# Optimization experiments

Measured on AMD Instinct MI355X. Metric: run time of the kernel, lower is better.

The kernel has to match this reference:

```python
import jax, jax.numpy as jnp
import numpy as np

EPS = 1e-12  # matches torch F.normalize default eps


def setup_inputs() -> dict:
    key = jax.random.key(0)
    k_x, k_w1, k_b1, k_w2, k_b2 = jax.random.split(key, 5)
    b, n, r, d = 8, 64, 256, 512
    return {
        "x": jax.random.normal(k_x, (b, n, r, d), dtype=jnp.float32),
        "W1": jax.random.normal(k_w1, (d, d), dtype=jnp.float32) * (1.0 / np.sqrt(d)),
        "b1": jax.random.normal(k_b1, (d,), dtype=jnp.float32) * 0.01,
        "W2": jax.random.normal(k_w2, (1, d), dtype=jnp.float32) * (1.0 / np.sqrt(d)),
        "b2": jax.random.normal(k_b2, (1,), dtype=jnp.float32) * 0.01,
    }


def reference(x, W1, b1, W2, b2):
    # F.normalize(x, dim=-1): x / max(||x||_2, eps)
    norm = jnp.sqrt(jnp.sum(x * x, axis=-1, keepdims=True))
    xn = x / jnp.maximum(norm, EPS)                      # [b,n,r,d]
    h = jnp.tanh(jnp.einsum('bnrd,ed->bnre', xn, W1) + b1)  # linear1 + tanh
    scores = (jnp.einsum('bnrd,od->bnro', h, W2) + b2)[..., 0]  # [b,n,r]
    alphas = jax.nn.softmax(scores, axis=2)              # softmax over regions r
    fbar = jnp.einsum('bnr,bnrd->bnd', alphas, xn)       # weighted pooling
    return (fbar, alphas)
```

## Files before the change

kernel.cpp:

```cpp
#include <hip/hip_runtime.h>
#include <hip/hip_bf16.h>

typedef short short8 __attribute__((ext_vector_type(8)));
typedef float floatx4 __attribute__((ext_vector_type(4)));

#define NGROUP 512
#define RREG 256
#define D 512
#define ROWS 131072
#define FBAR_ELEMS (NGROUP * D)

__device__ __forceinline__ unsigned short f2bf(float f) {
    unsigned int u = __float_as_uint(f);
    unsigned int r = (u + 0x7fffu + ((u >> 16) & 1u)) >> 16;
    return (unsigned short)r;
}
__device__ __forceinline__ float fast_tanh(float x) {
    float cx = fminf(fmaxf(x, -9.5f), 9.5f);
    float e  = __builtin_amdgcn_exp2f(cx * 2.8853900817779268f);
    return (e - 1.f) * __builtin_amdgcn_rcpf(e + 1.f);
}

__global__ __launch_bounds__(256) void conv_w1(const float* __restrict__ W1,
                                               unsigned short* __restrict__ W1c) {
    int tid = blockIdx.x * 256 + threadIdx.x;
    int P = tid * 8;
    int kc = P >> 15;
    int L = P & 32767;
    int col = L >> 6;
    int q = L & 63;
    int kl = (q ^ (((col >> 1) & 3) << 4)) >> 1;
    const float* src = W1 + col * 512 + kc * 32 + kl;
    float4 v = *reinterpret_cast<const float4*>(src);
    ushort4 o;
    o.x = f2bf(v.x); o.y = f2bf(v.y); o.z = f2bf(v.z); o.w = f2bf(v.w);
    *reinterpret_cast<ushort4*>((char*)W1c + P) = o;
}

__global__ __launch_bounds__(512, 4) void score_gemm(
    const float* __restrict__ x, const unsigned short* __restrict__ W1c,
    const float* __restrict__ b1, const float* __restrict__ W2v,
    float* __restrict__ inv_norm, float* __restrict__ scores) {

    __shared__ unsigned short A_lds[2][64 * 32];
    __shared__ unsigned short B_lds[2][512 * 32];
    __shared__ float ss_lds[64][8];
    __shared__ float inv_s[64];
    __shared__ float scorebuf[8][64];

    const int t = threadIdx.x;
    const int lane = t & 63;
    const int w = t >> 6;
    const int cl = lane & 15;
    const int hi = lane >> 4;
    const size_t row0 = (size_t)blockIdx.x * 64;

    auto stageB = [&](int buf, int kc) {
        const char* gb = (const char*)W1c + kc * 32768 + w * 4096 + lane * 16;
        char* lb = (char*)B_lds[buf] + w * 4096;
        #pragma unroll
        for (int i = 0; i < 4; ++i) {
            __builtin_amdgcn_global_load_lds(
                (const __attribute__((address_space(1))) void*)(gb + i * 1024),
                (__attribute__((address_space(3))) void*)(lb + i * 1024),
                16, 0, 0);
        }
    };

    const int arow = t >> 3;
    const int abyte = arow * 64 + (((t & 7) * 8) ^ (((arow >> 1) & 3) << 4));
    const float* xbase = x + (row0 + arow) * (size_t)D + (t & 7) * 4;

    float ssacc = 0.f;
    auto packA = [&](int buf, const float4& xv) {
        ssacc += xv.x * xv.x + xv.y * xv.y + xv.z * xv.z + xv.w * xv.w;
        ushort4 pk;
        pk.x = f2bf(xv.x); pk.y = f2bf(xv.y); pk.z = f2bf(xv.z); pk.w = f2bf(xv.w);
        *reinterpret_cast<ushort4*>((char*)A_lds[buf] + abyte) = pk;
    };

    stageB(0, 0);
    {
        float4 xv = *reinterpret_cast<const float4*>(xbase);
        packA(0, xv);
    }
    __syncthreads();

    floatx4 acc[4][4];
    #pragma unroll
    for (int tt = 0; tt < 4; ++tt)
        #pragma unroll
        for (int f = 0; f < 4; ++f) acc[tt][f] = floatx4{0, 0, 0, 0};

    const int fswz = ((cl >> 1) & 3) << 4;
    const int fofs = (hi * 16) ^ fswz;

    #pragma unroll 2
    for (int s = 0; s < 16; ++s) {
        const int cur = s & 1, nx = cur ^ 1;

        float4 xv;
        if (s < 15) {
            xv = *reinterpret_cast<const float4*>(xbase + (s + 1) * 32);
            stageB(nx, s + 1);
        }

        short8 afr[4], bfr[4];
        #pragma unroll
        for (int tt = 0; tt < 4; ++tt)
            afr[tt] = *reinterpret_cast<const short8*>(
                (char*)A_lds[cur] + (tt * 16 + cl) * 64 + fofs);
        #pragma unroll
        for (int f = 0; f < 4; ++f)
            bfr[f] = *reinterpret_cast<const short8*>(
                (char*)B_lds[cur] + (w * 64 + f * 16 + cl) * 64 + fofs);

        #pragma unroll
        for (int tt = 0; tt < 4; ++tt)
            #pragma unroll
            for (int f = 0; f < 4; ++f)
                acc[tt][f] = __builtin_amdgcn_mfma_f32_16x16x32_bf16(
                    afr[tt], bfr[f], acc[tt][f], 0, 0, 0);

        if (s < 15) {
            packA(nx, xv);
            __syncthreads();
        }
    }

    ss_lds[arow][t & 7] = ssacc;
    __syncthreads();
    if (t < 64) {
        float ss = 0.f;
        #pragma unroll
        for (int j = 0; j < 8; ++j) ss += ss_lds[t][j];
        float inv = 1.0f / fmaxf(sqrtf(ss), 1e-12f);
        inv_s[t] = inv;
        inv_norm[row0 + t] = inv;
    }
    __syncthreads();

    float sp[4][4];
    #pragma unroll
    for (int tt = 0; tt < 4; ++tt)
        #pragma unroll
        for (int i = 0; i < 4; ++i) sp[tt][i] = 0.f;

    #pragma unroll
    for (int f = 0; f < 4; ++f) {
        int col = w * 64 + f * 16 + cl;
        float wv = W2v[col];
        float bb = b1[col];
        #pragma unroll
        for (int tt = 0; tt < 4; ++tt) {
            #pragma unroll
            for (int i = 0; i < 4; ++i) {
                float iv = inv_s[tt * 16 + hi * 4 + i];
                sp[tt][i] += wv * fast_tanh(acc[tt][f][i] * iv + bb);
            }
        }
    }

    #pragma unroll
    for (int tt = 0; tt < 4; ++tt) {
        #pragma unroll
        for (int i = 0; i < 4; ++i) {
            float v = sp[tt][i];
            v += __shfl_xor(v, 1, 64);
            v += __shfl_xor(v, 2, 64);
            v += __shfl_xor(v, 4, 64);
            v += __shfl_xor(v, 8, 64);
            if (cl == 0) scorebuf[w][tt * 16 + hi * 4 + i] = v;
        }
    }
    __syncthreads();

    if (t < 64) {
        float s = 0.f;
        #pragma unroll
        for (int q = 0; q < 8; ++q) s += scorebuf[q][t];
        scores[row0 + t] = s;
    }
}

__global__ __launch_bounds__(512) void softmax_pool(
    const float* __restrict__ x, const float* __restrict__ inv_norm,
    const float* __restrict__ scores, float* __restrict__ out) {

    __shared__ float F[RREG];
    __shared__ float wts[RREG];
    const int t = threadIdx.x;
    const int g = blockIdx.x;

    float s = 0.f, e = 0.f;
    if (t < RREG) { s = scores[g * RREG + t]; F[t] = s; }
    __syncthreads();
    for (int off = 128; off > 0; off >>= 1) {
        if (t < off) F[t] = fmaxf(F[t], F[t + off]);
        __syncthreads();
    }
    float mx = F[0];
    __syncthreads();
    if (t < RREG) { e = expf(s - mx); F[t] = e; }
    __syncthreads();
    for (int off = 128; off > 0; off >>= 1) {
        if (t < off) F[t] += F[t + off];
        __syncthreads();
    }
    float denom = F[0];
    if (t < RREG) {
        float al = e / denom;
        out[FBAR_ELEMS + (size_t)g * RREG + t] = al;
        wts[t] = al * inv_norm[(size_t)g * RREG + t];
    }
    __syncthreads();

    float a = 0.f;
    const float* xb = x + (size_t)g * RREG * D + t;
    #pragma unroll 16
    for (int r = 0; r < RREG; ++r) a += wts[r] * xb[(size_t)r * D];
    out[(size_t)g * D + t] = a;
}

extern "C" void kernel_launch(void* const* d_in, const int* in_sizes, int n_in,
                              void* d_out, int out_size, void* d_ws, size_t ws_size,
                              hipStream_t stream) {
    const float* x  = (const float*)d_in[0];
    const float* W1 = (const float*)d_in[1];
    const float* b1 = (const float*)d_in[2];
    const float* w2 = (const float*)d_in[3];
    float* out = (float*)d_out;

    unsigned short* W1c = (unsigned short*)d_ws;
    float* inv_norm = (float*)((char*)d_ws + 524288);
    float* scores   = (float*)((char*)d_ws + 1048576);

    conv_w1<<<256, 256, 0, stream>>>(W1, W1c);
    score_gemm<<<ROWS / 64, 512, 0, stream>>>(x, W1c, b1, w2, inv_norm, scores);
    softmax_pool<<<NGROUP, 512, 0, stream>>>(x, inv_norm, scores, out);
}
```

Before: 160.1 us.

## Double score GEMM block to 1024 threads with 32 columns per wave

The score GEMM block grows from 512 to 1024 threads (16 waves), so each wave now computes 64 rows by 32 columns instead of 64 columns. The A-tile load and the W1 staging are split across twice as many threads. The row sum-of-squares reduction now uses 16-lane shuffles instead of an LDS pass, and the score buffer reuses the A LDS region to save shared memory. The aim is more waves per CU to hide memory latency and fewer registers per thread. The cost is half as many MFMAs per LDS fragment load and more block-wide synchronisation overhead.

```diff
diff --git a/kernel.cpp b/kernel.cpp
--- a/kernel.cpp
+++ b/kernel.cpp
@@ -37,16 +37,14 @@
     *reinterpret_cast<ushort4*>((char*)W1c + P) = o;
 }
 
-__global__ __launch_bounds__(512, 4) void score_gemm(
+__global__ __launch_bounds__(1024, 8) void score_gemm(
     const float* __restrict__ x, const unsigned short* __restrict__ W1c,
     const float* __restrict__ b1, const float* __restrict__ W2v,
     float* __restrict__ inv_norm, float* __restrict__ scores) {
 
     __shared__ unsigned short A_lds[2][64 * 32];
     __shared__ unsigned short B_lds[2][512 * 32];
-    __shared__ float ss_lds[64][8];
     __shared__ float inv_s[64];
-    __shared__ float scorebuf[8][64];
 
     const int t = threadIdx.x;
     const int lane = t & 63;
@@ -56,10 +54,10 @@
     const size_t row0 = (size_t)blockIdx.x * 64;
 
     auto stageB = [&](int buf, int kc) {
-        const char* gb = (const char*)W1c + kc * 32768 + w * 4096 + lane * 16;
-        char* lb = (char*)B_lds[buf] + w * 4096;
-        #pragma unroll
-        for (int i = 0; i < 4; ++i) {
+        const char* gb = (const char*)W1c + kc * 32768 + w * 2048 + lane * 16;
+        char* lb = (char*)B_lds[buf] + w * 2048;
+        #pragma unroll
+        for (int i = 0; i < 2; ++i) {
             __builtin_amdgcn_global_load_lds(
                 (const __attribute__((address_space(1))) void*)(gb + i * 1024),
                 (__attribute__((address_space(3))) void*)(lb + i * 1024),
@@ -67,60 +65,52 @@
         }
     };
 
-    const int arow = t >> 3;
-    const int abyte = arow * 64 + (((t & 7) * 8) ^ (((arow >> 1) & 3) << 4));
-    const float* xbase = x + (row0 + arow) * (size_t)D + (t & 7) * 4;
+    const int arow = t >> 4;
+    const int kq = t & 15;
+    const int abyte = arow * 64 + ((kq * 4) ^ (((arow >> 1) & 3) << 4));
+    const float* xp = x + (row0 + arow) * (size_t)D + kq * 2;
 
     float ssacc = 0.f;
-    auto packA = [&](int buf, const float4& xv) {
-        ssacc += xv.x * xv.x + xv.y * xv.y + xv.z * xv.z + xv.w * xv.w;
-        ushort4 pk;
-        pk.x = f2bf(xv.x); pk.y = f2bf(xv.y); pk.z = f2bf(xv.z); pk.w = f2bf(xv.w);
-        *reinterpret_cast<ushort4*>((char*)A_lds[buf] + abyte) = pk;
+    auto packA = [&](int buf, float2 v) {
+        ssacc += v.x * v.x + v.y * v.y;
+        unsigned int pk = (unsigned int)f2bf(v.x) | ((unsigned int)f2bf(v.y) << 16);
+        *reinterpret_cast<unsigned int*>((char*)A_lds[buf] + abyte) = pk;
     };
 
     stageB(0, 0);
-    {
-        float4 xv = *reinterpret_cast<const float4*>(xbase);
-        packA(0, xv);
-    }
-    __syncthreads();
-
-    floatx4 acc[4][4];
+    packA(0, *reinterpret_cast<const float2*>(xp));
+    __syncthreads();
+
+    floatx4 acc[4][2];
     #pragma unroll
-    for (int tt = 0; tt < 4; ++tt)
-        #pragma unroll
-        for (int f = 0; f < 4; ++f) acc[tt][f] = floatx4{0, 0, 0, 0};
-
-    const int fswz = ((cl >> 1) & 3) << 4;
-    const int fofs = (hi * 16) ^ fswz;
+    for (int tt = 0; tt < 4; ++tt) {
+        acc[tt][0] = floatx4{0, 0, 0, 0};
+        acc[tt][1] = floatx4{0, 0, 0, 0};
+    }
+
+    const int fofs = (hi * 16) ^ (((cl >> 1) & 3) << 4);
 
     #pragma unroll 2
     for (int s = 0; s < 16; ++s) {
         const int cur = s & 1, nx = cur ^ 1;
 
-        float4 xv;
+        float2 xv;
         if (s < 15) {
-            xv = *reinterpret_cast<const float4*>(xbase + (s + 1) * 32);
+            xv = *reinterpret_cast<const float2*>(xp + (s + 1) * 32);
             stageB(nx, s + 1);
         }
 
-        short8 afr[4], bfr[4];
-        #pragma unroll
-        for (int tt = 0; tt < 4; ++tt)
-            afr[tt] = *reinterpret_cast<const short8*>(
+        short8 bfr0 = *reinterpret_cast<const short8*>(
+            (char*)B_lds[cur] + (w * 32 + cl) * 64 + fofs);
+        short8 bfr1 = *reinterpret_cast<const short8*>(
+            (char*)B_lds[cur] + (w * 32 + 16 + cl) * 64 + fofs);
+        #pragma unroll
+        for (int tt = 0; tt < 4; ++tt) {
+            short8 afr = *reinterpret_cast<const short8*>(
                 (char*)A_lds[cur] + (tt * 16 + cl) * 64 + fofs);
-        #pragma unroll
-        for (int f = 0; f < 4; ++f)
-            bfr[f] = *reinterpret_cast<const short8*>(
-                (char*)B_lds[cur] + (w * 64 + f * 16 + cl) * 64 + fofs);
-
-        #pragma unroll
-        for (int tt = 0; tt < 4; ++tt)
-            #pragma unroll
-            for (int f = 0; f < 4; ++f)
-                acc[tt][f] = __builtin_amdgcn_mfma_f32_16x16x32_bf16(
-                    afr[tt], bfr[f], acc[tt][f], 0, 0, 0);
+            acc[tt][0] = __builtin_amdgcn_mfma_f32_16x16x32_bf16(afr, bfr0, acc[tt][0], 0, 0, 0);
+            acc[tt][1] = __builtin_amdgcn_mfma_f32_16x16x32_bf16(afr, bfr1, acc[tt][1], 0, 0, 0);
+        }
 
         if (s < 15) {
             packA(nx, xv);
@@ -128,49 +118,40 @@
         }
     }
 
-    ss_lds[arow][t & 7] = ssacc;
-    __syncthreads();
-    if (t < 64) {
-        float ss = 0.f;
-        #pragma unroll
-        for (int j = 0; j < 8; ++j) ss += ss_lds[t][j];
-        float inv = 1.0f / fmaxf(sqrtf(ss), 1e-12f);
-        inv_s[t] = inv;
-        inv_norm[row0 + t] = inv;
-    }
-    __syncthreads();
-
-    float sp[4][4];
-    #pragma unroll
-    for (int tt = 0; tt < 4; ++tt)
-        #pragma unroll
-        for (int i = 0; i < 4; ++i) sp[tt][i] = 0.f;
-
-    #pragma unroll
-    for (int f = 0; f < 4; ++f) {
-        int col = w * 64 + f * 16 + cl;
-        float wv = W2v[col];
-        float bb = b1[col];
-        #pragma unroll
-        for (int tt = 0; tt < 4; ++tt) {
-            #pragma unroll
-            for (int i = 0; i < 4; ++i) {
-                float iv = inv_s[tt * 16 + hi * 4 + i];
-                sp[tt][i] += wv * fast_tanh(acc[tt][f][i] * iv + bb);
-            }
-        }
-    }
+    ssacc += __shfl_xor(ssacc, 1, 16);
+    ssacc += __shfl_xor(ssacc, 2, 16);
+    ssacc += __shfl_xor(ssacc, 4, 16);
+    ssacc += __shfl_xor(ssacc, 8, 16);
+    if (kq == 0) {
+        float inv = 1.0f / fmaxf(sqrtf(ssacc), 1e-12f);
+        inv_s[arow] = inv;
+        inv_norm[row0 + arow] = inv;
+    }
+    __syncthreads();
+
+    float* scorebuf = (float*)A_lds;
 
     #pragma unroll
     for (int tt = 0; tt < 4; ++tt) {
+        floatx4 iv = *reinterpret_cast<const floatx4*>(&inv_s[tt * 16 + hi * 4]);
+        float sp[4] = {0.f, 0.f, 0.f, 0.f};
+        #pragma unroll
+        for (int f = 0; f < 2; ++f) {
+            int col = w * 32 + f * 16 + cl;
+            float wv = W2v[col];
+            float bb = b1[col];
+            #pragma unroll
+            for (int i = 0; i < 4; ++i)
+                sp[i] += wv * fast_tanh(acc[tt][f][i] * iv[i] + bb);
+        }
         #pragma unroll
         for (int i = 0; i < 4; ++i) {
-            float v = sp[tt][i];
+            float v = sp[i];
             v += __shfl_xor(v, 1, 64);
             v += __shfl_xor(v, 2, 64);
             v += __shfl_xor(v, 4, 64);
             v += __shfl_xor(v, 8, 64);
-            if (cl == 0) scorebuf[w][tt * 16 + hi * 4 + i] = v;
+            if (cl == 0) scorebuf[w * 64 + tt * 16 + hi * 4 + i] = v;
         }
     }
     __syncthreads();
@@ -178,7 +159,7 @@
     if (t < 64) {
         float s = 0.f;
         #pragma unroll
-        for (int q = 0; q < 8; ++q) s += scorebuf[q][t];
+        for (int q = 0; q < 16; ++q) s += scorebuf[q * 64 + t];
         scores[row0 + t] = s;
     }
 }
@@ -236,6 +217,6 @@
     float* scores   = (float*)((char*)d_ws + 1048576);
 
     conv_w1<<<256, 256, 0, stream>>>(W1, W1c);
-    score_gemm<<<ROWS / 64, 512, 0, stream>>>(x, W1c, b1, w2, inv_norm, scores);
+    score_gemm<<<ROWS / 64, 1024, 0, stream>>>(x, W1c, b1, w2, inv_norm, scores);
     softmax_pool<<<NGROUP, 512, 0, stream>>>(x, inv_norm, scores, out);
 }
```

Measured after the change: 163.9 us. +2.4%, slower.

## Prefetch x two stages ahead with manual waitcnt and barrier control

Applied to the files above, without the earlier changes.

Restructures the score GEMM main loop so x rows are loaded two K-steps ahead into rotating registers. Explicit s_waitcnt vmcnt counts replace the compiler's full waits, so the MFMA work overlaps the outstanding global and LDS-DMA loads, and the last iterations are peeled. The aim is to hide global load latency in the memory-bound x stream. The cost is more live registers, and correctness now depends on the hand-tuned vmcnt values matching the number of issued loads.

```diff
diff --git a/kernel.cpp b/kernel.cpp
--- a/kernel.cpp
+++ b/kernel.cpp
@@ -80,10 +80,9 @@
     };
 
     stageB(0, 0);
-    {
-        float4 xv = *reinterpret_cast<const float4*>(xbase);
-        packA(0, xv);
-    }
+    float4 xr0 = *reinterpret_cast<const float4*>(xbase);
+    float4 xr1 = *reinterpret_cast<const float4*>(xbase + 32);
+    packA(0, xr0);
     __syncthreads();
 
     floatx4 acc[4][4];
@@ -92,19 +91,9 @@
         #pragma unroll
         for (int f = 0; f < 4; ++f) acc[tt][f] = floatx4{0, 0, 0, 0};
 
-    const int fswz = ((cl >> 1) & 3) << 4;
-    const int fofs = (hi * 16) ^ fswz;
-
-    #pragma unroll 2
-    for (int s = 0; s < 16; ++s) {
-        const int cur = s & 1, nx = cur ^ 1;
-
-        float4 xv;
-        if (s < 15) {
-            xv = *reinterpret_cast<const float4*>(xbase + (s + 1) * 32);
-            stageB(nx, s + 1);
-        }
-
+    const int fofs = (hi * 16) ^ (((cl >> 1) & 3) << 4);
+
+    auto compute = [&](int cur) {
         short8 afr[4], bfr[4];
         #pragma unroll
         for (int tt = 0; tt < 4; ++tt)
@@ -114,18 +103,35 @@
         for (int f = 0; f < 4; ++f)
             bfr[f] = *reinterpret_cast<const short8*>(
                 (char*)B_lds[cur] + (w * 64 + f * 16 + cl) * 64 + fofs);
-
         #pragma unroll
         for (int tt = 0; tt < 4; ++tt)
             #pragma unroll
             for (int f = 0; f < 4; ++f)
                 acc[tt][f] = __builtin_amdgcn_mfma_f32_16x16x32_bf16(
                     afr[tt], bfr[f], acc[tt][f], 0, 0, 0);
-
-        if (s < 15) {
-            packA(nx, xv);
-            __syncthreads();
-        }
+    };
+
+    #pragma unroll 2
+    for (int s = 0; s < 14; ++s) {
+        const int cur = s & 1, nx = cur ^ 1;
+        float4 xn = *reinterpret_cast<const float4*>(xbase + (s + 2) * 32);
+        stageB(nx, s + 1);
+        asm volatile("s_waitcnt vmcnt(5)" ::: "memory");
+        compute(cur);
+        packA(nx, (s & 1) ? xr0 : xr1);
+        if (s & 1) xr1 = xn; else xr0 = xn;
+        asm volatile("s_waitcnt lgkmcnt(0)\ns_barrier" ::: "memory");
+    }
+    {
+        stageB(1, 15);
+        asm volatile("s_waitcnt vmcnt(4)" ::: "memory");
+        compute(0);
+        packA(1, xr1);
+        asm volatile("s_waitcnt lgkmcnt(0)\ns_barrier" ::: "memory");
+    }
+    {
+        asm volatile("s_waitcnt vmcnt(0)" ::: "memory");
+        compute(1);
     }
 
     ss_lds[arow][t & 7] = ssacc;
```

New measurement: 153.0 us. 1.05x faster.
